# Kernel tuning notes

Hardware: AMD Instinct MI355X
Metric: run time of the kernel (lower is better)

## Reference

```python
import jax, jax.numpy as jnp
import numpy as np

B, C, D, H = 4, 1024, 768, 12      # batch, seq_len(>512 long-doc), hidden, heads
E, K, S, V, P = 32, 2, 24, 8, 512  # entities, mentions/entity, sents, virtual nodes, ht pairs
NT = 256                            # node type embedding dim
EMB, BLK, NL = 768, 64, 97          # emb_size, block_size, num_labels
OFFSET = 1


def setup_inputs() -> dict:
    key = jax.random.key(0)
    ks = jax.random.split(key, 13)
    return {
        "sequence_output": jax.random.normal(ks[0], (B, C, D), jnp.float32),
        "attention": jax.random.uniform(ks[1], (B, H, C, C), jnp.float32),
        "entity_pos": jax.random.randint(ks[2], (B, E, K), 0, C - 2),
        "sent_pos": jax.random.randint(ks[3], (B, S), 0, C - 2),
        "virtual_pos": jax.random.randint(ks[4], (B, V), 0, C - 2),
        "hts": jax.random.randint(ks[5], (B, P, 2), 0, E),
        "node_type_emb": jax.random.normal(ks[6], (B, E, NT), jnp.float32) * 0.02,
        "W_head": jax.random.normal(ks[7], (2 * D + NT, EMB), jnp.float32) * 0.02,
        "b_head": jnp.zeros((EMB,), jnp.float32),
        "W_tail": jax.random.normal(ks[8], (2 * D + NT, EMB), jnp.float32) * 0.02,
        "b_tail": jnp.zeros((EMB,), jnp.float32),
        "W_bil": jax.random.normal(ks[9], (EMB * BLK, NL), jnp.float32) * 0.02,
        "b_bil": jnp.zeros((NL,), jnp.float32),
    }


def reference(sequence_output, attention, entity_pos, sent_pos, virtual_pos, hts,
              node_type_emb, W_head, b_head, W_tail, b_tail, W_bil, b_bil):
    # --- get_mention_embed / get_entity_embed: gather mention-start rows ---
    idx = entity_pos + OFFSET                      # [B,E,K] token index of each mention start
    flat = idx.reshape(B, E * K)                   # mention order matches torch double loop
    mention_embed = jnp.take_along_axis(sequence_output, flat[:, :, None], axis=1)  # [B,E*K,D]
    entity_embed = jax.nn.logsumexp(mention_embed.reshape(B, E, K, D), axis=2)      # [B,E,D]

    # --- get_sent_embed / get_virtual_embed: single-row gathers ---
    sent_embed = jnp.take_along_axis(sequence_output, (sent_pos + OFFSET)[:, :, None], axis=1)      # [B,S,D]
    virtual_embed = jnp.take_along_axis(sequence_output, (virtual_pos + OFFSET)[:, :, None], axis=1)  # [B,V,D]

    # --- get_rss: localized-context pooling over attention ---
    att_t = attention.transpose(0, 2, 1, 3)        # [B,C,H,C] so we gather query rows
    e_att = jnp.take_along_axis(att_t, flat[:, :, None, None], axis=1)  # [B,E*K,H,C]
    e_att = e_att.reshape(B, E, K, H, C).mean(axis=2)                   # [B,E,H,C] mean over mentions
    h_att = jnp.take_along_axis(e_att, hts[:, :, 0][:, :, None, None], axis=1)  # [B,P,H,C]
    t_att = jnp.take_along_axis(e_att, hts[:, :, 1][:, :, None, None], axis=1)  # [B,P,H,C]
    ht_att = (h_att * t_att).mean(axis=2)                               # [B,P,C] mean over heads
    ht_att = ht_att / (ht_att.sum(axis=-1, keepdims=True) + 1e-5)
    rs = jnp.einsum('bld,brl->brd', sequence_output, ht_att)            # [B,P,D]

    # --- get_pair_entity_embed on entity hidden state (entity_embed + node-type emb) ---
    ent_hidden = jnp.concatenate([entity_embed, node_type_emb], axis=-1)          # [B,E,D+NT]
    s_emb = jnp.take_along_axis(ent_hidden, hts[:, :, 0][:, :, None], axis=1)     # [B,P,D+NT]
    t_emb = jnp.take_along_axis(ent_hidden, hts[:, :, 1][:, :, None], axis=1)

    # --- head/tail extractors + grouped bilinear classifier ---
    hs = jnp.tanh(jnp.concatenate([s_emb, rs], axis=-1) @ W_head + b_head)  # [B,P,EMB]
    ts = jnp.tanh(jnp.concatenate([t_emb, rs], axis=-1) @ W_tail + b_tail)
    b1 = hs.reshape(B, P, EMB // BLK, BLK)
    b2 = ts.reshape(B, P, EMB // BLK, BLK)
    bl = (b1[..., :, None] * b2[..., None, :]).reshape(B, P, EMB * BLK)     # [B,P,EMB*BLK]
    logits = bl @ W_bil + b_bil                                             # [B,P,NL]
    return (logits, mention_embed, sent_embed, virtual_embed)
```

## Files before the change

kernel.cpp:

```cpp
#include <hip/hip_runtime.h>

#define B_   4
#define C_   1024
#define D_   768
#define H_   12
#define E_   32
#define K_   2
#define S_   24
#define V_   8
#define P_   512
#define NT_  256
#define EMB_ 768
#define BLK_ 64
#define NL_  97
#define DNT_ 1024
#define KHT_ 1792
#define KBIL_ 49152
#define NPAD_ 128

typedef __bf16 bf16x8 __attribute__((ext_vector_type(8)));
typedef float  f32x4  __attribute__((ext_vector_type(4)));

__device__ __forceinline__ float b2f(unsigned short u) {
    return (float)__builtin_bit_cast(__bf16, u);
}
__device__ __forceinline__ unsigned short f2b(float f) {
    return __builtin_bit_cast(unsigned short, (__bf16)f);
}
__device__ __forceinline__ float ld_in(const void* p, size_t i, int isf) {
    return isf ? ((const float*)p)[i] : b2f(((const unsigned short*)p)[i]);
}
__device__ __forceinline__ void st_out(void* p, size_t i, float v, int isf) {
    if (isf) ((float*)p)[i] = v;
    else     ((unsigned short*)p)[i] = f2b(v);
}

__global__ __launch_bounds__(256) void k_probe(const unsigned short* __restrict__ seq_u,
                                               int* __restrict__ flag)
{
    __shared__ int sh_huge[256];
    __shared__ int sh_zero[256];
    int tid = threadIdx.x;
    int huge = 0, zero = 0;
    for (int i = tid; i < 4096; i += 256) {
        unsigned short u = seq_u[2 * i];
        float f = b2f(u);
        if (!(fabsf(f) <= 1e10f)) huge = 1;
        if (u == 0) zero++;
    }
    sh_huge[tid] = huge; sh_zero[tid] = zero;
    __syncthreads();
    for (int s = 128; s > 0; s >>= 1) {
        if (tid < s) { sh_huge[tid] |= sh_huge[tid + s]; sh_zero[tid] += sh_zero[tid + s]; }
        __syncthreads();
    }
    if (tid == 0) flag[0] = (sh_huge[0] || sh_zero[0] > 3600) ? 1 : 0;
}

#define PREP_GATHER 256
#define PREP_EATT   (PREP_GATHER + B_*E_*H_)
#define PREP_TSEQ   (PREP_EATT + 768)
#define PREP_TW     (PREP_TSEQ + 672)
#define PREP_TBIL   (PREP_TW + 768)

__global__ __launch_bounds__(256) void k_prep(
    const void* __restrict__ seq, const void* __restrict__ att,
    const int* __restrict__ epos, const int* __restrict__ spos,
    const int* __restrict__ vpos, const void* __restrict__ ntype,
    const void* __restrict__ Wh, const void* __restrict__ Wt_,
    const void* __restrict__ Wb,
    float* __restrict__ enth, float* __restrict__ e_att,
    unsigned short* __restrict__ seqT,
    unsigned short* __restrict__ WtH, unsigned short* __restrict__ WtT,
    unsigned short* __restrict__ WtB,
    void* __restrict__ outv, long long moff, long long soff, long long voff,
    const int* __restrict__ dflag)
{
    __shared__ __align__(16) unsigned char smem[12544];
    int blk = blockIdx.x, tid = threadIdx.x;
    int isf = *dflag;
    if (blk < PREP_GATHER) {
        if (blk < B_ * E_) {
            int b = blk / E_, e = blk % E_;
            int i0 = epos[(b * E_ + e) * K_ + 0] + 1;
            int i1 = epos[(b * E_ + e) * K_ + 1] + 1;
            size_t r0 = ((size_t)b * C_ + i0) * D_;
            size_t r1 = ((size_t)b * C_ + i1) * D_;
            size_t m0 = (size_t)moff + ((size_t)(b * E_ * K_) + 2 * e) * D_;
            size_t m1 = m0 + D_;
            float* eh = enth + (size_t)(b * E_ + e) * DNT_;
            for (int d = tid; d < D_; d += 256) {
                float a = ld_in(seq, r0 + d, isf);
                float c = ld_in(seq, r1 + d, isf);
                st_out(outv, m0 + d, a, isf);
                st_out(outv, m1 + d, c, isf);
                float mx = fmaxf(a, c);
                eh[d] = mx + logf(expf(a - mx) + expf(c - mx));
            }
            size_t nt0 = (size_t)(b * E_ + e) * NT_;
            for (int j = tid; j < NT_; j += 256) eh[D_ + j] = ld_in(ntype, nt0 + j, isf);
        } else if (blk < B_ * E_ + B_ * S_) {
            int t = blk - B_ * E_; int b = t / S_, s = t % S_;
            int i = spos[b * S_ + s] + 1;
            size_t r = ((size_t)b * C_ + i) * D_;
            size_t o = (size_t)soff + (size_t)(b * S_ + s) * D_;
            for (int d = tid; d < D_; d += 256) st_out(outv, o + d, ld_in(seq, r + d, isf), isf);
        } else {
            int t = blk - B_ * E_ - B_ * S_; int b = t / V_, v = t % V_;
            int i = vpos[b * V_ + v] + 1;
            size_t r = ((size_t)b * C_ + i) * D_;
            size_t o = (size_t)voff + (size_t)(b * V_ + v) * D_;
            for (int d = tid; d < D_; d += 256) st_out(outv, o + d, ld_in(seq, r + d, isf), isf);
        }
    } else if (blk < PREP_EATT) {
        int t = blk - PREP_GATHER;
        int b = t / (E_ * H_); int r = t % (E_ * H_); int e = r / H_; int h = r % H_;
        int i0 = epos[(b * E_ + e) * K_ + 0] + 1;
        int i1 = epos[(b * E_ + e) * K_ + 1] + 1;
        size_t a0 = (((size_t)b * H_ + h) * C_ + i0) * C_;
        size_t a1 = (((size_t)b * H_ + h) * C_ + i1) * C_;
        float* o = e_att + (((size_t)(b * E_ + e)) * H_ + h) * C_;
        for (int c = tid; c < C_; c += 256)
            o[c] = 0.5f * (ld_in(att, a0 + c, isf) + ld_in(att, a1 + c, isf));
    } else if (blk < PREP_TSEQ) {
        int t = blk - PREP_EATT;
        int b = t / 192; int r = t % 192; int ct = r / 12; int dt = r % 12;
        typedef unsigned short row65[65];
        row65* tile = (row65*)smem;
        for (int idx = tid; idx < 4096; idx += 256) {
            int cc = idx >> 6, dd = idx & 63;
            tile[cc][dd] = f2b(ld_in(seq, ((size_t)b * C_ + ct * 64 + cc) * D_ + dt * 64 + dd, isf));
        }
        __syncthreads();
        for (int idx = tid; idx < 4096; idx += 256) {
            int dd = idx >> 6, cc = idx & 63;
            seqT[((size_t)b * D_ + dt * 64 + dd) * C_ + ct * 64 + cc] = tile[cc][dd];
        }
    } else if (blk < PREP_TW) {
        int t = blk - PREP_TSEQ;
        int mat = t / 336; int r = t % 336; int kt = r / 12; int nt = r % 12;
        const void* in = mat ? Wt_ : Wh;
        unsigned short* out = mat ? WtT : WtH;
        typedef unsigned short row65[65];
        row65* tile = (row65*)smem;
        for (int idx = tid; idx < 4096; idx += 256) {
            int kk = idx >> 6, nn = idx & 63;
            tile[kk][nn] = f2b(ld_in(in, ((size_t)kt * 64 + kk) * EMB_ + nt * 64 + nn, isf));
        }
        __syncthreads();
        for (int idx = tid; idx < 4096; idx += 256) {
            int nn = idx >> 6, kk = idx & 63;
            out[((size_t)nt * 64 + nn) * KHT_ + kt * 64 + kk] = tile[kk][nn];
        }
    } else {
        int t = blk - PREP_TW;
        int k0 = t << 6;
        unsigned short* raw = (unsigned short*)smem;
        for (int idx = tid; idx < 64 * NL_; idx += 256)
            raw[idx] = f2b(ld_in(Wb, (size_t)k0 * NL_ + idx, isf));
        __syncthreads();
        int kk = tid & 63, nq = tid >> 6;
        for (int i = 0; i < 32; i++) {
            int n = nq * 32 + i;
            unsigned short v = (n < NL_) ? raw[kk * NL_ + n] : (unsigned short)0;
            WtB[(size_t)n * KBIL_ + k0 + kk] = v;
        }
    }
}

__global__ __launch_bounds__(256) void k_mid(
    const float* __restrict__ e_att, const float* __restrict__ enth,
    const int* __restrict__ hts,
    unsigned short* __restrict__ htb,
    unsigned short* __restrict__ Xh, unsigned short* __restrict__ Xt)
{
    __shared__ float red[4];
    int blk = blockIdx.x, tid = threadIdx.x;
    if (blk < B_ * P_) {
        int b = blk >> 9;
        int he = hts[blk * 2 + 0], te = hts[blk * 2 + 1];
        const float* ph = e_att + (size_t)(b * E_ + he) * H_ * C_;
        const float* pt = e_att + (size_t)(b * E_ + te) * H_ * C_;
        float v[4]; float ls = 0.f;
        for (int ci = 0; ci < 4; ci++) {
            int c = tid + (ci << 8);
            float acc = 0.f;
#pragma unroll
            for (int h = 0; h < H_; h++) acc += ph[h * C_ + c] * pt[h * C_ + c];
            acc *= (1.0f / (float)H_);
            v[ci] = acc; ls += acc;
        }
        for (int off = 32; off > 0; off >>= 1) ls += __shfl_down(ls, off, 64);
        if ((tid & 63) == 0) red[tid >> 6] = ls;
        __syncthreads();
        float inv = 1.0f / (red[0] + red[1] + red[2] + red[3] + 1e-5f);
        for (int ci = 0; ci < 4; ci++)
            htb[((size_t)blk << 10) + tid + (ci << 8)] = f2b(v[ci] * inv);
    } else {
        int m = blk - B_ * P_; int b = m >> 9;
        int eh = hts[m * 2 + 0], et = hts[m * 2 + 1];
        const float* sh = enth + (size_t)(b * E_ + eh) * DNT_;
        const float* st = enth + (size_t)(b * E_ + et) * DNT_;
        for (int k = tid; k < DNT_; k += 256) {
            Xh[(size_t)m * KHT_ + k] = f2b(sh[k]);
            Xt[(size_t)m * KHT_ + k] = f2b(st[k]);
        }
    }
}

__global__ __launch_bounds__(256) void k_zero(float* __restrict__ p) {
    ((float4*)p)[(size_t)blockIdx.x * 256 + threadIdx.x] = make_float4(0.f, 0.f, 0.f, 0.f);
}

__global__ __launch_bounds__(256) void k_gemm(
    const unsigned short* __restrict__ A0, const unsigned short* __restrict__ A1,
    const unsigned short* __restrict__ B0, const unsigned short* __restrict__ B1,
    long long lda, long long ldb, long long sAz, long long sBz,
    int nsteps, int zmode,
    float* __restrict__ outF0, float* __restrict__ outF1,
    unsigned short* __restrict__ oX1, unsigned short* __restrict__ oX2)
{
    int n0 = blockIdx.x * 64, m0 = blockIdx.y * 64, z = blockIdx.z;
    const unsigned short* Ab; const unsigned short* Bb;
    float* outF = nullptr; int kc0 = 0;
    if (zmode == 0) {
        Ab = A0 + (size_t)z * sAz; Bb = B0 + (size_t)z * sBz;
    } else {
        int mat = z >> 1, kh = z & 1;
        Ab = mat ? A1 : A0; Bb = mat ? B1 : B0;
        outF = mat ? outF1 : outF0;
        kc0 = kh * (nsteps * 32);
    }
    __shared__ __align__(16) unsigned short a_lds[64][40];
    __shared__ __align__(16) unsigned short b_lds[64][40];
    int tid = threadIdx.x, lane = tid & 63, w = tid >> 6;
    int wm = (w >> 1) * 32, wn = (w & 1) * 32, q = lane >> 4, l15 = lane & 15;
    f32x4 acc00 = {0.f,0.f,0.f,0.f}, acc01 = acc00, acc10 = acc00, acc11 = acc00;
    int srow = tid >> 2, sch = (tid & 3) * 8;
    const unsigned short* pa = Ab + (size_t)(m0 + srow) * lda + kc0 + sch;
    const unsigned short* pb = Bb + (size_t)(n0 + srow) * ldb + kc0 + sch;
    int4 ra = *(const int4*)pa;
    int4 rb = *(const int4*)pb;
    for (int ks = 0; ks < nsteps; ks++) {
        __syncthreads();
        *(int4*)&a_lds[srow][sch] = ra;
        *(int4*)&b_lds[srow][sch] = rb;
        __syncthreads();
        if (ks + 1 < nsteps) {
            ra = *(const int4*)(pa + (size_t)(ks + 1) * 32);
            rb = *(const int4*)(pb + (size_t)(ks + 1) * 32);
        }
        bf16x8 a0 = *(const bf16x8*)&a_lds[wm + l15][q * 8];
        bf16x8 a1 = *(const bf16x8*)&a_lds[wm + 16 + l15][q * 8];
        bf16x8 b0 = *(const bf16x8*)&b_lds[wn + l15][q * 8];
        bf16x8 b1 = *(const bf16x8*)&b_lds[wn + 16 + l15][q * 8];
        acc00 = __builtin_amdgcn_mfma_f32_16x16x32_bf16(a0, b0, acc00, 0, 0, 0);
        acc01 = __builtin_amdgcn_mfma_f32_16x16x32_bf16(a0, b1, acc01, 0, 0, 0);
        acc10 = __builtin_amdgcn_mfma_f32_16x16x32_bf16(a1, b0, acc10, 0, 0, 0);
        acc11 = __builtin_amdgcn_mfma_f32_16x16x32_bf16(a1, b1, acc11, 0, 0, 0);
    }
    f32x4 accs[2][2] = {{acc00, acc01}, {acc10, acc11}};
#pragma unroll
    for (int mt = 0; mt < 2; mt++)
#pragma unroll
        for (int nt = 0; nt < 2; nt++) {
            int gmb = m0 + wm + mt * 16 + q * 4;
            int gn  = n0 + wn + nt * 16 + l15;
            if (zmode == 0) {
#pragma unroll
                for (int r = 0; r < 4; r++) {
                    unsigned short v = f2b(accs[mt][nt][r]);
                    size_t o = (size_t)(z * P_ + gmb + r) * KHT_ + DNT_ + gn;
                    oX1[o] = v; oX2[o] = v;
                }
            } else {
#pragma unroll
                for (int r = 0; r < 4; r++)
                    atomicAdd(&outF[(size_t)(gmb + r) * EMB_ + gn], accs[mt][nt][r]);
            }
        }
}

__global__ __launch_bounds__(256) void k_bil(
    const float* __restrict__ hsF, const float* __restrict__ tsF,
    const void* __restrict__ b_head, const void* __restrict__ b_tail,
    const unsigned short* __restrict__ WtB, float* __restrict__ logitsF,
    const int* __restrict__ dflag)
{
    int m0 = blockIdx.x * 32;
    int g  = blockIdx.y;
    int isf = *dflag;
    int tid = threadIdx.x, lane = tid & 63, w = tid >> 6;
    int q = lane >> 4, l15 = lane & 15;
    __shared__ __align__(16) float hsl[32][68];
    __shared__ __align__(16) float tsl[32][68];
    for (int idx = tid; idx < 2048; idx += 256) {
        int m = idx >> 6, j = idx & 63;
        int col = g * 64 + j;
        float bh = ld_in(b_head, col, isf);
        float bt = ld_in(b_tail, col, isf);
        hsl[m][j] = tanhf(hsF[(size_t)(m0 + m) * EMB_ + col] + bh);
        tsl[m][j] = tanhf(tsF[(size_t)(m0 + m) * EMB_ + col] + bt);
    }
    __syncthreads();

    const unsigned short* pB0 = WtB + (size_t)(w * 16 + l15) * KBIL_ + g * 4096 + q * 8;
    const unsigned short* pB1 = pB0 + (size_t)64 * KBIL_;
    bf16x8 rb0[2], rb1[2];
    rb0[0] = *(const bf16x8*)(pB0);      rb1[0] = *(const bf16x8*)(pB1);
    rb0[1] = *(const bf16x8*)(pB0 + 32); rb1[1] = *(const bf16x8*)(pB1 + 32);
    f32x4 acc00 = {0.f,0.f,0.f,0.f}, acc01 = acc00, acc10 = acc00, acc11 = acc00;

#pragma unroll 2
    for (int kk = 0; kk < 128; kk++) {
        int sl = kk & 1;
        bf16x8 bw0 = rb0[sl], bw1 = rb1[sl];
        if (kk + 2 < 128) {
            rb0[sl] = *(const bf16x8*)(pB0 + (size_t)(kk + 2) * 32);
            rb1[sl] = *(const bf16x8*)(pB1 + (size_t)(kk + 2) * 32);
        }
        int i = kk >> 1, h = kk & 1;
        float ha0 = hsl[l15][i];
        float ha1 = hsl[16 + l15][i];
        const float4* t0p = (const float4*)&tsl[l15][h * 32 + q * 8];
        const float4* t1p = (const float4*)&tsl[16 + l15][h * 32 + q * 8];
        float4 t0a = t0p[0], t0b = t0p[1];
        float4 t1a = t1p[0], t1b = t1p[1];
        bf16x8 af0, af1;
        af0[0] = (__bf16)(ha0 * t0a.x); af0[1] = (__bf16)(ha0 * t0a.y);
        af0[2] = (__bf16)(ha0 * t0a.z); af0[3] = (__bf16)(ha0 * t0a.w);
        af0[4] = (__bf16)(ha0 * t0b.x); af0[5] = (__bf16)(ha0 * t0b.y);
        af0[6] = (__bf16)(ha0 * t0b.z); af0[7] = (__bf16)(ha0 * t0b.w);
        af1[0] = (__bf16)(ha1 * t1a.x); af1[1] = (__bf16)(ha1 * t1a.y);
        af1[2] = (__bf16)(ha1 * t1a.z); af1[3] = (__bf16)(ha1 * t1a.w);
        af1[4] = (__bf16)(ha1 * t1b.x); af1[5] = (__bf16)(ha1 * t1b.y);
        af1[6] = (__bf16)(ha1 * t1b.z); af1[7] = (__bf16)(ha1 * t1b.w);
        acc00 = __builtin_amdgcn_mfma_f32_16x16x32_bf16(af0, bw0, acc00, 0, 0, 0);
        acc01 = __builtin_amdgcn_mfma_f32_16x16x32_bf16(af0, bw1, acc01, 0, 0, 0);
        acc10 = __builtin_amdgcn_mfma_f32_16x16x32_bf16(af1, bw0, acc10, 0, 0, 0);
        acc11 = __builtin_amdgcn_mfma_f32_16x16x32_bf16(af1, bw1, acc11, 0, 0, 0);
    }
#pragma unroll
    for (int r = 0; r < 4; r++) {
        atomicAdd(&logitsF[(size_t)(m0 + q * 4 + r) * NPAD_ + w * 16 + l15],           acc00[r]);
        atomicAdd(&logitsF[(size_t)(m0 + q * 4 + r) * NPAD_ + w * 16 + 64 + l15],      acc01[r]);
        atomicAdd(&logitsF[(size_t)(m0 + 16 + q * 4 + r) * NPAD_ + w * 16 + l15],      acc10[r]);
        atomicAdd(&logitsF[(size_t)(m0 + 16 + q * 4 + r) * NPAD_ + w * 16 + 64 + l15], acc11[r]);
    }
}

__global__ __launch_bounds__(256) void k_fin(
    const float* __restrict__ logitsF, const void* __restrict__ b_bil,
    void* __restrict__ outv, const int* __restrict__ dflag)
{
    int isf = *dflag;
    int idx = blockIdx.x * 256 + threadIdx.x;
    if (idx >= B_ * P_ * NL_) return;
    int m = idx / NL_, n = idx % NL_;
    st_out(outv, idx, logitsF[(size_t)m * NPAD_ + n] + ld_in(b_bil, n, isf), isf);
}

extern "C" void kernel_launch(void* const* d_in, const int* in_sizes, int n_in,
                              void* d_out, int out_size, void* d_ws, size_t ws_size,
                              hipStream_t stream)
{
    const void* seq    = d_in[0];
    const void* att    = d_in[1];
    const int*  epos   = (const int*)d_in[2];
    const int*  spos   = (const int*)d_in[3];
    const int*  vpos   = (const int*)d_in[4];
    const int*  hts    = (const int*)d_in[5];
    const void* ntype  = d_in[6];
    const void* W_head = d_in[7];
    const void* b_head = d_in[8];
    const void* W_tail = d_in[9];
    const void* b_tail = d_in[10];
    const void* W_bil  = d_in[11];
    const void* b_bil  = d_in[12];

    long long mention_off = (long long)B_ * P_ * NL_;
    long long sent_off    = mention_off + (long long)B_ * E_ * K_ * D_;
    long long virt_off    = sent_off + (long long)B_ * S_ * D_;

    char* p = (char*)d_ws;
    auto alloc = [&](size_t bytes) { void* r = (void*)p; p += (bytes + 255) & ~(size_t)255; return r; };
    int*            dflag   = (int*)alloc(256);
    float*          e_att   = (float*)alloc((size_t)B_ * E_ * H_ * C_ * 4);
    unsigned short* htb     = (unsigned short*)alloc((size_t)B_ * P_ * C_ * 2);
    unsigned short* seqT    = (unsigned short*)alloc((size_t)B_ * D_ * C_ * 2);
    unsigned short* WtH     = (unsigned short*)alloc((size_t)EMB_ * KHT_ * 2);
    unsigned short* WtT     = (unsigned short*)alloc((size_t)EMB_ * KHT_ * 2);
    unsigned short* WtB     = (unsigned short*)alloc((size_t)NPAD_ * KBIL_ * 2);
    unsigned short* Xh      = (unsigned short*)alloc((size_t)B_ * P_ * KHT_ * 2);
    unsigned short* Xt      = (unsigned short*)alloc((size_t)B_ * P_ * KHT_ * 2);
    float*          hsF     = (float*)alloc((size_t)B_ * P_ * EMB_ * 4);
    float*          tsF     = (float*)alloc((size_t)B_ * P_ * EMB_ * 4);
    float*          logitsF = (float*)alloc((size_t)B_ * P_ * NPAD_ * 4);
    float*          enth    = (float*)alloc((size_t)B_ * E_ * DNT_ * 4);

    dim3 blk(256);
    k_probe<<<1, blk, 0, stream>>>((const unsigned short*)seq, dflag);
    k_prep<<<PREP_TBIL, blk, 0, stream>>>(
        seq, att, epos, spos, vpos, ntype, W_head, W_tail, W_bil,
        enth, e_att, seqT, WtH, WtT, WtB,
        d_out, mention_off, sent_off, virt_off, dflag);
    k_mid<<<2 * B_ * P_, blk, 0, stream>>>(e_att, enth, hts, htb, Xh, Xt);
    k_zero<<<3328, blk, 0, stream>>>(hsF);
    k_gemm<<<dim3(EMB_ / 64, P_ / 64, B_), blk, 0, stream>>>(
        htb, nullptr, seqT, nullptr, C_, C_,
        (long long)P_ * C_, (long long)D_ * C_, C_ / 32, 0,
        nullptr, nullptr, Xh, Xt);
    k_gemm<<<dim3(EMB_ / 64, (B_ * P_) / 64, 4), blk, 0, stream>>>(
        Xh, Xt, WtH, WtT, KHT_, KHT_, 0, 0, KHT_ / 64, 1,
        hsF, tsF, nullptr, nullptr);
    k_bil<<<dim3((B_ * P_) / 32, 12, 1), blk, 0, stream>>>(
        hsF, tsF, b_head, b_tail, WtB, logitsF, dflag);
    k_fin<<<(B_ * P_ * NL_ + 255) / 256, blk, 0, stream>>>(logitsF, b_bil, d_out, dflag);
}
```

Before: 473.1 us.

## Fuse bias+tanh into head/tail GEMM epilogue, drop split-K atomics, store bf16

The head/tail GEMM no longer splits K in two with fp32 atomicAdd into zeroed buffers. Each block now runs the full K, applies bias and tanh in its epilogue, and writes bf16 hs/ts directly. The bilinear kernel loads these bf16 tiles instead of recomputing tanh from fp32, and zeroing of the logits buffer is folded into k_mid as extra blocks, removing the separate k_zero launch. The aim is to cut atomics, a launch and fp32 traffic, at the cost of half as many GEMM blocks with twice the K loop, which lowers parallelism.

```diff
diff --git a/kernel.cpp b/kernel.cpp
--- a/kernel.cpp
+++ b/kernel.cpp
@@ -172,7 +172,8 @@
     const float* __restrict__ e_att, const float* __restrict__ enth,
     const int* __restrict__ hts,
     unsigned short* __restrict__ htb,
-    unsigned short* __restrict__ Xh, unsigned short* __restrict__ Xt)
+    unsigned short* __restrict__ Xh, unsigned short* __restrict__ Xt,
+    float* __restrict__ logitsF)
 {
     __shared__ float red[4];
     int blk = blockIdx.x, tid = threadIdx.x;
@@ -196,7 +197,7 @@
         float inv = 1.0f / (red[0] + red[1] + red[2] + red[3] + 1e-5f);
         for (int ci = 0; ci < 4; ci++)
             htb[((size_t)blk << 10) + tid + (ci << 8)] = f2b(v[ci] * inv);
-    } else {
+    } else if (blk < 2 * B_ * P_) {
         int m = blk - B_ * P_; int b = m >> 9;
         int eh = hts[m * 2 + 0], et = hts[m * 2 + 1];
         const float* sh = enth + (size_t)(b * E_ + eh) * DNT_;
@@ -205,11 +206,10 @@
             Xh[(size_t)m * KHT_ + k] = f2b(sh[k]);
             Xt[(size_t)m * KHT_ + k] = f2b(st[k]);
         }
-    }
-}
-
-__global__ __launch_bounds__(256) void k_zero(float* __restrict__ p) {
-    ((float4*)p)[(size_t)blockIdx.x * 256 + threadIdx.x] = make_float4(0.f, 0.f, 0.f, 0.f);
+    } else {
+        int t = blk - 2 * B_ * P_;
+        ((float4*)logitsF)[(size_t)t * 256 + tid] = make_float4(0.f, 0.f, 0.f, 0.f);
+    }
 }
 
 __global__ __launch_bounds__(256) void k_gemm(
@@ -217,19 +217,19 @@
     const unsigned short* __restrict__ B0, const unsigned short* __restrict__ B1,
     long long lda, long long ldb, long long sAz, long long sBz,
     int nsteps, int zmode,
-    float* __restrict__ outF0, float* __restrict__ outF1,
-    unsigned short* __restrict__ oX1, unsigned short* __restrict__ oX2)
+    const void* __restrict__ bias0, const void* __restrict__ bias1,
+    unsigned short* __restrict__ oY0, unsigned short* __restrict__ oY1,
+    unsigned short* __restrict__ oX1, unsigned short* __restrict__ oX2,
+    const int* __restrict__ dflag)
 {
     int n0 = blockIdx.x * 64, m0 = blockIdx.y * 64, z = blockIdx.z;
     const unsigned short* Ab; const unsigned short* Bb;
-    float* outF = nullptr; int kc0 = 0;
+    unsigned short* oY = nullptr; const void* bias = nullptr;
     if (zmode == 0) {
         Ab = A0 + (size_t)z * sAz; Bb = B0 + (size_t)z * sBz;
     } else {
-        int mat = z >> 1, kh = z & 1;
-        Ab = mat ? A1 : A0; Bb = mat ? B1 : B0;
-        outF = mat ? outF1 : outF0;
-        kc0 = kh * (nsteps * 32);
+        Ab = z ? A1 : A0; Bb = z ? B1 : B0;
+        oY = z ? oY1 : oY0; bias = z ? bias1 : bias0;
     }
     __shared__ __align__(16) unsigned short a_lds[64][40];
     __shared__ __align__(16) unsigned short b_lds[64][40];
@@ -237,8 +237,8 @@
     int wm = (w >> 1) * 32, wn = (w & 1) * 32, q = lane >> 4, l15 = lane & 15;
     f32x4 acc00 = {0.f,0.f,0.f,0.f}, acc01 = acc00, acc10 = acc00, acc11 = acc00;
     int srow = tid >> 2, sch = (tid & 3) * 8;
-    const unsigned short* pa = Ab + (size_t)(m0 + srow) * lda + kc0 + sch;
-    const unsigned short* pb = Bb + (size_t)(n0 + srow) * ldb + kc0 + sch;
+    const unsigned short* pa = Ab + (size_t)(m0 + srow) * lda + sch;
+    const unsigned short* pb = Bb + (size_t)(n0 + srow) * ldb + sch;
     int4 ra = *(const int4*)pa;
     int4 rb = *(const int4*)pb;
     for (int ks = 0; ks < nsteps; ks++) {
@@ -260,6 +260,7 @@
         acc11 = __builtin_amdgcn_mfma_f32_16x16x32_bf16(a1, b1, acc11, 0, 0, 0);
     }
     f32x4 accs[2][2] = {{acc00, acc01}, {acc10, acc11}};
+    int isf = (zmode == 1) ? *dflag : 0;
 #pragma unroll
     for (int mt = 0; mt < 2; mt++)
 #pragma unroll
@@ -274,33 +275,28 @@
                     oX1[o] = v; oX2[o] = v;
                 }
             } else {
+                float bv = ld_in(bias, gn, isf);
 #pragma unroll
                 for (int r = 0; r < 4; r++)
-                    atomicAdd(&outF[(size_t)(gmb + r) * EMB_ + gn], accs[mt][nt][r]);
+                    oY[(size_t)(gmb + r) * EMB_ + gn] = f2b(tanhf(accs[mt][nt][r] + bv));
             }
         }
 }
 
 __global__ __launch_bounds__(256) void k_bil(
-    const float* __restrict__ hsF, const float* __restrict__ tsF,
-    const void* __restrict__ b_head, const void* __restrict__ b_tail,
-    const unsigned short* __restrict__ WtB, float* __restrict__ logitsF,
-    const int* __restrict__ dflag)
+    const unsigned short* __restrict__ hsB, const unsigned short* __restrict__ tsB,
+    const unsigned short* __restrict__ WtB, float* __restrict__ logitsF)
 {
     int m0 = blockIdx.x * 32;
     int g  = blockIdx.y;
-    int isf = *dflag;
     int tid = threadIdx.x, lane = tid & 63, w = tid >> 6;
     int q = lane >> 4, l15 = lane & 15;
-    __shared__ __align__(16) float hsl[32][68];
-    __shared__ __align__(16) float tsl[32][68];
-    for (int idx = tid; idx < 2048; idx += 256) {
-        int m = idx >> 6, j = idx & 63;
-        int col = g * 64 + j;
-        float bh = ld_in(b_head, col, isf);
-        float bt = ld_in(b_tail, col, isf);
-        hsl[m][j] = tanhf(hsF[(size_t)(m0 + m) * EMB_ + col] + bh);
-        tsl[m][j] = tanhf(tsF[(size_t)(m0 + m) * EMB_ + col] + bt);
+    __shared__ __align__(16) unsigned short hsl[32][80];
+    __shared__ __align__(16) unsigned short tsl[32][80];
+    for (int idx = tid; idx < 512; idx += 256) {
+        int m = idx >> 4, j4 = (idx & 15) * 4;
+        *(ushort4*)&hsl[m][j4] = *(const ushort4*)&hsB[(size_t)(m0 + m) * EMB_ + g * 64 + j4];
+        *(ushort4*)&tsl[m][j4] = *(const ushort4*)&tsB[(size_t)(m0 + m) * EMB_ + g * 64 + j4];
     }
     __syncthreads();
 
@@ -320,21 +316,16 @@
             rb1[sl] = *(const bf16x8*)(pB1 + (size_t)(kk + 2) * 32);
         }
         int i = kk >> 1, h = kk & 1;
-        float ha0 = hsl[l15][i];
-        float ha1 = hsl[16 + l15][i];
-        const float4* t0p = (const float4*)&tsl[l15][h * 32 + q * 8];
-        const float4* t1p = (const float4*)&tsl[16 + l15][h * 32 + q * 8];
-        float4 t0a = t0p[0], t0b = t0p[1];
-        float4 t1a = t1p[0], t1b = t1p[1];
+        float ha0 = b2f(hsl[l15][i]);
+        float ha1 = b2f(hsl[16 + l15][i]);
+        bf16x8 t0 = *(const bf16x8*)&tsl[l15][h * 32 + q * 8];
+        bf16x8 t1 = *(const bf16x8*)&tsl[16 + l15][h * 32 + q * 8];
         bf16x8 af0, af1;
-        af0[0] = (__bf16)(ha0 * t0a.x); af0[1] = (__bf16)(ha0 * t0a.y);
-        af0[2] = (__bf16)(ha0 * t0a.z); af0[3] = (__bf16)(ha0 * t0a.w);
-        af0[4] = (__bf16)(ha0 * t0b.x); af0[5] = (__bf16)(ha0 * t0b.y);
-        af0[6] = (__bf16)(ha0 * t0b.z); af0[7] = (__bf16)(ha0 * t0b.w);
-        af1[0] = (__bf16)(ha1 * t1a.x); af1[1] = (__bf16)(ha1 * t1a.y);
-        af1[2] = (__bf16)(ha1 * t1a.z); af1[3] = (__bf16)(ha1 * t1a.w);
-        af1[4] = (__bf16)(ha1 * t1b.x); af1[5] = (__bf16)(ha1 * t1b.y);
-        af1[6] = (__bf16)(ha1 * t1b.z); af1[7] = (__bf16)(ha1 * t1b.w);
+#pragma unroll
+        for (int j = 0; j < 8; j++) {
+            af0[j] = (__bf16)(ha0 * (float)t0[j]);
+            af1[j] = (__bf16)(ha1 * (float)t1[j]);
+        }
         acc00 = __builtin_amdgcn_mfma_f32_16x16x32_bf16(af0, bw0, acc00, 0, 0, 0);
         acc01 = __builtin_amdgcn_mfma_f32_16x16x32_bf16(af0, bw1, acc01, 0, 0, 0);
         acc10 = __builtin_amdgcn_mfma_f32_16x16x32_bf16(af1, bw0, acc10, 0, 0, 0);
@@ -393,8 +384,8 @@
     unsigned short* WtB     = (unsigned short*)alloc((size_t)NPAD_ * KBIL_ * 2);
     unsigned short* Xh      = (unsigned short*)alloc((size_t)B_ * P_ * KHT_ * 2);
     unsigned short* Xt      = (unsigned short*)alloc((size_t)B_ * P_ * KHT_ * 2);
-    float*          hsF     = (float*)alloc((size_t)B_ * P_ * EMB_ * 4);
-    float*          tsF     = (float*)alloc((size_t)B_ * P_ * EMB_ * 4);
+    unsigned short* hsB     = (unsigned short*)alloc((size_t)B_ * P_ * EMB_ * 2);
+    unsigned short* tsB     = (unsigned short*)alloc((size_t)B_ * P_ * EMB_ * 2);
     float*          logitsF = (float*)alloc((size_t)B_ * P_ * NPAD_ * 4);
     float*          enth    = (float*)alloc((size_t)B_ * E_ * DNT_ * 4);
 
@@ -404,16 +395,14 @@
         seq, att, epos, spos, vpos, ntype, W_head, W_tail, W_bil,
         enth, e_att, seqT, WtH, WtT, WtB,
         d_out, mention_off, sent_off, virt_off, dflag);
-    k_mid<<<2 * B_ * P_, blk, 0, stream>>>(e_att, enth, hts, htb, Xh, Xt);
-    k_zero<<<3328, blk, 0, stream>>>(hsF);
+    k_mid<<<2 * B_ * P_ + 256, blk, 0, stream>>>(e_att, enth, hts, htb, Xh, Xt, logitsF);
     k_gemm<<<dim3(EMB_ / 64, P_ / 64, B_), blk, 0, stream>>>(
         htb, nullptr, seqT, nullptr, C_, C_,
         (long long)P_ * C_, (long long)D_ * C_, C_ / 32, 0,
-        nullptr, nullptr, Xh, Xt);
-    k_gemm<<<dim3(EMB_ / 64, (B_ * P_) / 64, 4), blk, 0, stream>>>(
-        Xh, Xt, WtH, WtT, KHT_, KHT_, 0, 0, KHT_ / 64, 1,
-        hsF, tsF, nullptr, nullptr);
-    k_bil<<<dim3((B_ * P_) / 32, 12, 1), blk, 0, stream>>>(
-        hsF, tsF, b_head, b_tail, WtB, logitsF, dflag);
+        nullptr, nullptr, nullptr, nullptr, Xh, Xt, dflag);
+    k_gemm<<<dim3(EMB_ / 64, (B_ * P_) / 64, 2), blk, 0, stream>>>(
+        Xh, Xt, WtH, WtT, KHT_, KHT_, 0, 0, KHT_ / 32, 1,
+        b_head, b_tail, hsB, tsB, nullptr, nullptr, dflag);
+    k_bil<<<dim3((B_ * P_) / 32, 12, 1), blk, 0, stream>>>(hsB, tsB, WtB, logitsF);
     k_fin<<<(B_ * P_ * NL_ + 255) / 256, blk, 0, stream>>>(logitsF, b_bil, d_out, dflag);
 }
```

Result: faster. 453.9 us (-4.1%).
